# Kernel optimization log

Hardware: AMD Instinct MI355X
Metric: run time of the kernel (lower is better)

## Reference

```python
import jax, jax.numpy as jnp
import numpy as np

B, S, D = 4, 2048, 1024
H, HD = 16, 64  # num_head, head_dim


def setup_inputs() -> dict:
    key = jax.random.key(0)
    k0, k1, k2, k3, k4 = jax.random.split(key, 5)
    scale = 1.0 / np.sqrt(D)
    return {
        "x": jax.random.normal(k0, (B, S, D), dtype=jnp.float32),
        "Wq": jax.random.normal(k1, (D, H * HD), dtype=jnp.float32) * scale,
        "Wk": jax.random.normal(k2, (D, H * HD), dtype=jnp.float32) * scale,
        "Wv": jax.random.normal(k3, (D, H * HD), dtype=jnp.float32) * scale,
        "Wo": jax.random.normal(k4, (H * HD, H * HD), dtype=jnp.float32) * scale,
    }


def reference(x, Wq, Wk, Wv, Wo):
    b, s, _ = x.shape
    # projections -> [b, h, s, hd]
    q = (x @ Wq).reshape(b, s, H, HD).transpose(0, 2, 1, 3)
    k = (x @ Wk).reshape(b, s, H, HD).transpose(0, 2, 1, 3)
    v = (x @ Wv).reshape(b, s, H, HD).transpose(0, 2, 1, 3)
    # scaled scores [b, h, s, s]
    scores = jnp.einsum("bhqd,bhkd->bhqk", q, k) / np.sqrt(HD).astype(np.float32)
    causal = jnp.triu(jnp.ones((s, s), dtype=bool), k=1)  # True above diagonal
    scores = jnp.where(causal, -jnp.inf, scores)
    att = jax.nn.softmax(scores, axis=-1)
    # dropout p=0.0 -> identity
    out = jnp.einsum("bhqk,bhkd->bqhd", att, v).reshape(b, s, H * HD)
    return out @ Wo
```

## Files before the change

kernel.cpp:

```cpp
#include <hip/hip_runtime.h>


typedef __attribute__((ext_vector_type(8))) short short8_t;
typedef __attribute__((ext_vector_type(4))) short short4_t;
typedef __attribute__((ext_vector_type(4))) float float4_t;

constexpr int Bz = 4, Sq = 2048, Dm = 1024, NH = 16, HD = 64;

#define GLOAD_LDS16(g, l)                                                      \
  __builtin_amdgcn_global_load_lds(                                            \
      (const __attribute__((address_space(1))) unsigned int*)(g),              \
      (__attribute__((address_space(3))) unsigned int*)(l), 16, 0, 0)

__device__ __forceinline__ unsigned short f2bf(float f) {
  unsigned u = __builtin_bit_cast(unsigned, f);
  u += 0x7fffu + ((u >> 16) & 1u);
  return (unsigned short)(u >> 16);
}

__device__ __forceinline__ float exp2_fast(float x) {
#if __has_builtin(__builtin_amdgcn_exp2f)
  return __builtin_amdgcn_exp2f(x);
#else
  return exp2f(x);
#endif
}

__device__ __forceinline__ float m3(float a, float b, float c) {
  return fmaxf(fmaxf(a, b), c);
}

__global__ __launch_bounds__(256) void cast_x_kernel(const float* __restrict__ x,
                                                     unsigned short* __restrict__ xb) {
  size_t i = (size_t)blockIdx.x * 256 + threadIdx.x;
  float4 v = ((const float4*)x)[i];
  ushort4 o;
  o.x = f2bf(v.x); o.y = f2bf(v.y); o.z = f2bf(v.z); o.w = f2bf(v.w);
  ((ushort4*)xb)[i] = o;
}

__global__ __launch_bounds__(256) void transpose_w_kernel(
    const float* __restrict__ Wq, const float* __restrict__ Wk,
    const float* __restrict__ Wv, const float* __restrict__ Wo,
    unsigned short* __restrict__ wqT, unsigned short* __restrict__ wkT,
    unsigned short* __restrict__ wvT, unsigned short* __restrict__ woT) {
  __shared__ float tile[64][65];
  int zz = blockIdx.z;
  const float* W = zz == 0 ? Wq : (zz == 1 ? Wk : (zz == 2 ? Wv : Wo));
  unsigned short* WT = zz == 0 ? wqT : (zz == 1 ? wkT : (zz == 2 ? wvT : woT));
  int n0 = blockIdx.x * 64, k0 = blockIdx.y * 64;
  int tx = threadIdx.x & 63, ty = threadIdx.x >> 6;
#pragma unroll
  for (int i = 0; i < 16; ++i) {
    int r = i * 4 + ty;
    tile[r][tx] = W[(size_t)(k0 + r) * Dm + n0 + tx];
  }
  __syncthreads();
#pragma unroll
  for (int i = 0; i < 16; ++i) {
    int r = i * 4 + ty;
    WT[(size_t)(n0 + r) * Dm + k0 + tx] = f2bf(tile[tx][r]);
  }
}

__device__ __forceinline__ void gemm_mainloop(const unsigned short* __restrict__ A,
                                              const unsigned short* __restrict__ BT,
                                              int m0, int n0,
                                              unsigned short* lA, unsigned short* lB,
                                              float4_t acc[4][4]) {
  const int tid = threadIdx.x;
  const int lane = tid & 63, lr = lane & 15, quad = lane >> 4;
  const int wave = tid >> 6;
  const int mw = (wave >> 1) * 64, nw = (wave & 1) * 64;
  const int srow = tid >> 3;
  const int scol = (tid & 7) * 8;
  const unsigned short* ga = A + (size_t)(m0 + srow) * Dm + scol;
  const unsigned short* gb = BT + (size_t)(n0 + srow) * Dm + scol;
  unsigned short* la = lA + tid * 8;
  unsigned short* lb = lB + tid * 8;

  for (int k0 = 0; k0 < Dm; k0 += 64) {
    __syncthreads();
#pragma unroll
    for (int iss = 0; iss < 4; ++iss) {
      GLOAD_LDS16(ga + (size_t)iss * 32 * Dm + k0, la + iss * 32 * 64);
      GLOAD_LDS16(gb + (size_t)iss * 32 * Dm + k0, lb + iss * 32 * 64);
    }
    __syncthreads();
#pragma unroll
    for (int kk = 0; kk < 2; ++kk) {
      short8_t a[4], b[4];
#pragma unroll
      for (int i = 0; i < 4; ++i)
        a[i] = *(const short8_t*)(lA + (mw + i * 16 + lr) * 64 + kk * 32 + quad * 8);
#pragma unroll
      for (int j = 0; j < 4; ++j)
        b[j] = *(const short8_t*)(lB + (nw + j * 16 + lr) * 64 + kk * 32 + quad * 8);
#pragma unroll
      for (int i = 0; i < 4; ++i)
#pragma unroll
        for (int j = 0; j < 4; ++j)
          acc[i][j] = __builtin_amdgcn_mfma_f32_16x16x32_bf16(a[i], b[j], acc[i][j], 0, 0, 0);
    }
  }
}

__global__ __launch_bounds__(256) void gemm_qkv_kernel(
    const unsigned short* __restrict__ xb,
    const unsigned short* __restrict__ wqT, const unsigned short* __restrict__ wkT,
    const unsigned short* __restrict__ wvT,
    unsigned short* __restrict__ qb, unsigned short* __restrict__ kb,
    unsigned short* __restrict__ vt) {
  __shared__ unsigned short lA[128 * 64];
  __shared__ unsigned short lB[128 * 64];
  const unsigned short* WT = blockIdx.z == 0 ? wqT : (blockIdx.z == 1 ? wkT : wvT);
  unsigned short* outb = blockIdx.z == 0 ? qb : (blockIdx.z == 1 ? kb : vt);
  bool isV = blockIdx.z == 2;
  float qscale = (blockIdx.z == 0) ? 0.18033688011112042f : 1.0f;
  int lane = threadIdx.x & 63, wave = threadIdx.x >> 6;
  int lr = lane & 15, quad = lane >> 4;
  int m0 = blockIdx.y * 128, n0 = blockIdx.x * 128;
  int m_base = m0 + (wave >> 1) * 64;
  int n_base = n0 + (wave & 1) * 64;
  float4_t z = {0.f, 0.f, 0.f, 0.f};
  float4_t acc[4][4];
#pragma unroll
  for (int i = 0; i < 4; ++i)
#pragma unroll
    for (int j = 0; j < 4; ++j) acc[i][j] = z;
  gemm_mainloop(xb, WT, m0, n0, lA, lB, acc);
  if (isV) {
#pragma unroll
    for (int i = 0; i < 4; ++i)
#pragma unroll
      for (int j = 0; j < 4; ++j) {
        int m = m_base + i * 16 + quad * 4;
        int n = n_base + j * 16 + lr;
        int b = m >> 11, s = m & (Sq - 1);
        int h = n >> 6, hd = n & (HD - 1);
        ushort4 pk;
        pk.x = f2bf(acc[i][j][0]); pk.y = f2bf(acc[i][j][1]);
        pk.z = f2bf(acc[i][j][2]); pk.w = f2bf(acc[i][j][3]);
        *(ushort4*)(outb + (((size_t)b * NH + h) * HD + hd) * Sq + s) = pk;
      }
  } else {
#pragma unroll
    for (int i = 0; i < 4; ++i)
#pragma unroll
      for (int j = 0; j < 4; ++j)
#pragma unroll
        for (int r = 0; r < 4; ++r) {
          int m = m_base + i * 16 + quad * 4 + r;
          int n = n_base + j * 16 + lr;
          int b = m >> 11, s = m & (Sq - 1);
          int h = n >> 6, hd = n & (HD - 1);
          outb[(((size_t)b * NH + h) * Sq + s) * HD + hd] = f2bf(acc[i][j][r] * qscale);
        }
  }
}

__global__ __launch_bounds__(256) void gemm_out_kernel(
    const unsigned short* __restrict__ ao, const unsigned short* __restrict__ woT,
    float* __restrict__ out) {
  __shared__ unsigned short lA[128 * 64];
  __shared__ unsigned short lB[128 * 64];
  int lane = threadIdx.x & 63, wave = threadIdx.x >> 6;
  int lr = lane & 15, quad = lane >> 4;
  int m0 = blockIdx.y * 128, n0 = blockIdx.x * 128;
  int m_base = m0 + (wave >> 1) * 64;
  int n_base = n0 + (wave & 1) * 64;
  float4_t z = {0.f, 0.f, 0.f, 0.f};
  float4_t acc[4][4];
#pragma unroll
  for (int i = 0; i < 4; ++i)
#pragma unroll
    for (int j = 0; j < 4; ++j) acc[i][j] = z;
  gemm_mainloop(ao, woT, m0, n0, lA, lB, acc);
#pragma unroll
  for (int i = 0; i < 4; ++i)
#pragma unroll
    for (int j = 0; j < 4; ++j)
#pragma unroll
      for (int r = 0; r < 4; ++r) {
        int m = m_base + i * 16 + quad * 4 + r;
        int n = n_base + j * 16 + lr;
        out[(size_t)m * Dm + n] = acc[i][j][r];
      }
}

__global__ __launch_bounds__(256) void attn_kernel(
    const unsigned short* __restrict__ qbuf, const unsigned short* __restrict__ kbuf,
    const unsigned short* __restrict__ vtbuf, unsigned short* __restrict__ ao) {
  __shared__ unsigned short lk[64 * 64];
  __shared__ unsigned short lv[64 * 64];
  int tid = threadIdx.x;
  int bh = blockIdx.x;
  int ti = 31 - (int)blockIdx.y;
  int wave = tid >> 6, lane = tid & 63;
  int lcol = lane & 15, quad = lane >> 4;
  int lc7 = lcol & 7;
  const unsigned short* Q = qbuf + (size_t)bh * Sq * HD;
  const unsigned short* K = kbuf + (size_t)bh * Sq * HD;
  const unsigned short* Vt = vtbuf + (size_t)bh * HD * Sq;
  int b = bh >> 4, h = bh & 15;
  float4_t z = {0.f, 0.f, 0.f, 0.f};

  const int r0 = tid >> 3;
  const int sg = (tid & 7) ^ (r0 & 7);
  const unsigned short* kg_base = K + (size_t)r0 * HD + sg * 8;
  const unsigned short* vg_base = Vt + (size_t)r0 * Sq + sg * 8;
  unsigned short* kl0 = lk + tid * 8;
  unsigned short* kl1 = lk + 2048 + tid * 8;
  unsigned short* vl0 = lv + tid * 8;
  unsigned short* vl1 = lv + 2048 + tid * 8;

  const int koff0 = (quad ^ lc7) * 8;
  const int koff1 = ((quad | 4) ^ lc7) * 8;
  int voff[4];
#pragma unroll
  for (int s4 = 0; s4 < 4; ++s4)
    voff[s4] = (((s4 * 2 + (quad >> 1)) ^ lc7) * 8) + (quad & 1) * 4;

  int q0w = ti * 64 + wave * 16;
  int q_global = q0w + lcol;
  short8_t qf0 = *(const short8_t*)(Q + (size_t)(q0w + lcol) * HD + quad * 8);
  short8_t qf1 = *(const short8_t*)(Q + (size_t)(q0w + lcol) * HD + 32 + quad * 8);
  float m_i = -INFINITY, l_i = 0.f;
  float4_t o[4];
#pragma unroll
  for (int f = 0; f < 4; ++f) o[f] = z;

  int nkt = ti + 1;
  for (int kt = 0; kt < nkt; ++kt) {
    int key0 = kt * 64;
    __syncthreads();
    {
      const unsigned short* kg = kg_base + (size_t)key0 * HD;
      const unsigned short* vg = vg_base + key0;
      GLOAD_LDS16(kg, kl0);
      GLOAD_LDS16(kg + (size_t)32 * HD, kl1);
      GLOAD_LDS16(vg, vl0);
      GLOAD_LDS16(vg + (size_t)32 * Sq, vl1);
    }
    __syncthreads();

    bool need_mask = (key0 + 63 > q0w);
    float s[16];
#pragma unroll
    for (int s4 = 0; s4 < 4; ++s4) {
      const unsigned short* kr = lk + (s4 * 16 + lcol) * 64;
      short8_t kf0 = *(const short8_t*)(kr + koff0);
      short8_t kf1 = *(const short8_t*)(kr + koff1);
      float4_t st = z;
      st = __builtin_amdgcn_mfma_f32_16x16x32_bf16(kf0, qf0, st, 0, 0, 0);
      st = __builtin_amdgcn_mfma_f32_16x16x32_bf16(kf1, qf1, st, 0, 0, 0);
#pragma unroll
      for (int r = 0; r < 4; ++r) {
        float v = st[r];
        if (need_mask && (key0 + s4 * 16 + quad * 4 + r > q_global)) v = -INFINITY;
        s[s4 * 4 + r] = v;
      }
    }
    float ta = m3(s[0], s[1], s[2]);
    float tb = m3(s[3], s[4], s[5]);
    float tc = m3(s[6], s[7], s[8]);
    float td = m3(s[9], s[10], s[11]);
    float te = m3(s[12], s[13], s[14]);
    float tmax = m3(ta, tb, tc);
    tmax = m3(tmax, td, te);
    tmax = fmaxf(tmax, s[15]);
    tmax = fmaxf(tmax, __shfl_xor(tmax, 16, 64));
    tmax = fmaxf(tmax, __shfl_xor(tmax, 32, 64));

    if (__any(tmax > m_i + 8.f)) {
      float m_new = fmaxf(m_i, tmax);
      float alpha = exp2_fast(m_i - m_new);
      l_i *= alpha;
      m_i = m_new;
      float at[4];
#pragma unroll
      for (int r = 0; r < 4; ++r) at[r] = __shfl(alpha, quad * 4 + r, 64);
#pragma unroll
      for (int f = 0; f < 4; ++f)
#pragma unroll
        for (int r = 0; r < 4; ++r) o[f][r] *= at[r];
    }

    float psum = 0.f;
    short4_t pf[4];
#pragma unroll
    for (int s4 = 0; s4 < 4; ++s4) {
      float p0 = exp2_fast(s[s4 * 4 + 0] - m_i);
      float p1 = exp2_fast(s[s4 * 4 + 1] - m_i);
      float p2 = exp2_fast(s[s4 * 4 + 2] - m_i);
      float p3 = exp2_fast(s[s4 * 4 + 3] - m_i);
      psum += (p0 + p1) + (p2 + p3);
      unsigned lo, hi;
      asm("v_cvt_pk_bf16_f32 %0, %1, %2" : "=v"(lo) : "v"(p0), "v"(p1));
      asm("v_cvt_pk_bf16_f32 %0, %1, %2" : "=v"(hi) : "v"(p2), "v"(p3));
      uint2 packed;
      packed.x = lo;
      packed.y = hi;
      pf[s4] = __builtin_bit_cast(short4_t, packed);
    }
    psum += __shfl_xor(psum, 16, 64);
    psum += __shfl_xor(psum, 32, 64);
    l_i += psum;

#pragma unroll
    for (int f = 0; f < 4; ++f) {
      const unsigned short* vr = lv + (f * 16 + lcol) * 64;
#pragma unroll
      for (int s4 = 0; s4 < 4; ++s4) {
        short4_t vf = *(const short4_t*)(vr + voff[s4]);
        o[f] = __builtin_amdgcn_mfma_f32_16x16x16bf16_1k(pf[s4], vf, o[f], 0, 0, 0);
      }
    }
  }

  float lt[4];
#pragma unroll
  for (int r = 0; r < 4; ++r) lt[r] = 1.f / __shfl(l_i, quad * 4 + r, 64);
#pragma unroll
  for (int f = 0; f < 4; ++f)
#pragma unroll
    for (int r = 0; r < 4; ++r) {
      int q = q0w + quad * 4 + r;
      int hd = f * 16 + lcol;
      ao[((size_t)b * Sq + q) * (NH * HD) + h * HD + hd] = f2bf(o[f][r] * lt[r]);
    }
}

extern "C" void kernel_launch(void* const* d_in, const int* in_sizes, int n_in,
                              void* d_out, int out_size, void* d_ws, size_t ws_size,
                              hipStream_t stream) {
  const float* x = (const float*)d_in[0];
  const float* Wq = (const float*)d_in[1];
  const float* Wk = (const float*)d_in[2];
  const float* Wv = (const float*)d_in[3];
  const float* Wo = (const float*)d_in[4];
  float* out = (float*)d_out;

  char* ws = (char*)d_ws;
  size_t off = 0;
  auto carve = [&](size_t bytes) {
    void* p = ws + off;
    off += (bytes + 255) & ~(size_t)255;
    return p;
  };
  const size_t xe = (size_t)Bz * Sq * Dm;
  const size_t we = (size_t)Dm * Dm;
  unsigned short* xb = (unsigned short*)carve(xe * 2);
  unsigned short* wqT = (unsigned short*)carve(we * 2);
  unsigned short* wkT = (unsigned short*)carve(we * 2);
  unsigned short* wvT = (unsigned short*)carve(we * 2);
  unsigned short* woT = (unsigned short*)carve(we * 2);
  unsigned short* qb = (unsigned short*)carve(xe * 2);
  unsigned short* kb = (unsigned short*)carve(xe * 2);
  unsigned short* vt = (unsigned short*)carve(xe * 2);
  unsigned short* ao = (unsigned short*)carve(xe * 2);
  (void)ws_size;

  cast_x_kernel<<<xe / 4 / 256, 256, 0, stream>>>(x, xb);
  transpose_w_kernel<<<dim3(16, 16, 4), 256, 0, stream>>>(Wq, Wk, Wv, Wo,
                                                          wqT, wkT, wvT, woT);
  gemm_qkv_kernel<<<dim3(8, 64, 3), 256, 0, stream>>>(xb, wqT, wkT, wvT, qb, kb, vt);
  attn_kernel<<<dim3(Bz * NH, 32), 256, 0, stream>>>(qb, kb, vt, ao);
  gemm_out_kernel<<<dim3(8, 64), 256, 0, stream>>>(ao, woT, out);
}
```

Before: 280.6 us.

## Double-buffer K/V tiles in attention kernel with register-staged V prefetch

Attention now uses two LDS buffers for K and V, so the next key tile is prefetched while the current one is computed. This replaces the two barriers per iteration with one. K still uses async global-to-LDS loads, while V is loaded into registers early, stored to LDS with a new 8-byte-granularity XOR swizzle, and read with matching offsets. The causal mask is applied only on the diagonal tile. The cost is double the LDS use (which may lower occupancy) and more registers held for the staged V data.

```diff
diff --git a/kernel.cpp b/kernel.cpp
--- a/kernel.cpp
+++ b/kernel.cpp
@@ -191,8 +191,8 @@
 __global__ __launch_bounds__(256) void attn_kernel(
     const unsigned short* __restrict__ qbuf, const unsigned short* __restrict__ kbuf,
     const unsigned short* __restrict__ vtbuf, unsigned short* __restrict__ ao) {
-  __shared__ unsigned short lk[64 * 64];
-  __shared__ unsigned short lv[64 * 64];
+  __shared__ unsigned short lk[2 * 64 * 64];
+  __shared__ unsigned short lv[2 * 64 * 64];
   int tid = threadIdx.x;
   int bh = blockIdx.x;
   int ti = 31 - (int)blockIdx.y;
@@ -206,20 +206,26 @@
   float4_t z = {0.f, 0.f, 0.f, 0.f};
 
   const int r0 = tid >> 3;
-  const int sg = (tid & 7) ^ (r0 & 7);
-  const unsigned short* kg_base = K + (size_t)r0 * HD + sg * 8;
-  const unsigned short* vg_base = Vt + (size_t)r0 * Sq + sg * 8;
-  unsigned short* kl0 = lk + tid * 8;
-  unsigned short* kl1 = lk + 2048 + tid * 8;
-  unsigned short* vl0 = lv + tid * 8;
-  unsigned short* vl1 = lv + 2048 + tid * 8;
+  const int sgk = (tid & 7) ^ (r0 & 7);
+  const unsigned short* kg = K + (size_t)r0 * HD + sgk * 8;
+  const int kdst = tid * 8;
+
+  const int w0 = (tid & 7) * 2;
+  const int xa = r0 & 15;
+  const int d0 = w0 ^ xa;
+  const unsigned short* vsrc = Vt + (size_t)r0 * Sq + w0 * 4;
+  const int vdst = r0 * 64 + d0 * 4;
 
   const int koff0 = (quad ^ lc7) * 8;
   const int koff1 = ((quad | 4) ^ lc7) * 8;
   int voff[4];
 #pragma unroll
-  for (int s4 = 0; s4 < 4; ++s4)
-    voff[s4] = (((s4 * 2 + (quad >> 1)) ^ lc7) * 8) + (quad & 1) * 4;
+  for (int s4 = 0; s4 < 4; ++s4) voff[s4] = ((s4 * 4 + quad) ^ lcol) * 4;
+
+  unsigned short* lkc = lk;
+  unsigned short* lkn = lk + 4096;
+  unsigned short* lvc = lv;
+  unsigned short* lvn = lv + 4096;
 
   int q0w = ti * 64 + wave * 16;
   int q_global = q0w + lcol;
@@ -230,37 +236,56 @@
 #pragma unroll
   for (int f = 0; f < 4; ++f) o[f] = z;
 
+  {
+    GLOAD_LDS16(kg, lkc + kdst);
+    GLOAD_LDS16(kg + (size_t)32 * HD, lkc + 2048 + kdst);
+    short4_t a0 = *(const short4_t*)(vsrc);
+    short4_t a1 = *(const short4_t*)(vsrc + 4);
+    short4_t b0 = *(const short4_t*)(vsrc + (size_t)32 * Sq);
+    short4_t b1 = *(const short4_t*)(vsrc + (size_t)32 * Sq + 4);
+    *(short4_t*)(lvc + vdst) = a0;
+    *(short4_t*)(lvc + (vdst ^ 4)) = a1;
+    *(short4_t*)(lvc + vdst + 2048) = b0;
+    *(short4_t*)(lvc + (vdst ^ 4) + 2048) = b1;
+  }
+  __syncthreads();
+
   int nkt = ti + 1;
   for (int kt = 0; kt < nkt; ++kt) {
-    int key0 = kt * 64;
-    __syncthreads();
-    {
-      const unsigned short* kg = kg_base + (size_t)key0 * HD;
-      const unsigned short* vg = vg_base + key0;
-      GLOAD_LDS16(kg, kl0);
-      GLOAD_LDS16(kg + (size_t)32 * HD, kl1);
-      GLOAD_LDS16(vg, vl0);
-      GLOAD_LDS16(vg + (size_t)32 * Sq, vl1);
-    }
-    __syncthreads();
-
-    bool need_mask = (key0 + 63 > q0w);
+    bool has_next = (kt + 1 < nkt);
+    short4_t a0, a1, b0, b1;
+    if (has_next) {
+      const unsigned short* vs = vsrc + (size_t)(kt + 1) * 64;
+      a0 = *(const short4_t*)(vs);
+      a1 = *(const short4_t*)(vs + 4);
+      b0 = *(const short4_t*)(vs + (size_t)32 * Sq);
+      b1 = *(const short4_t*)(vs + (size_t)32 * Sq + 4);
+      const unsigned short* kgn = kg + (size_t)(kt + 1) * 64 * HD;
+      GLOAD_LDS16(kgn, lkn + kdst);
+      GLOAD_LDS16(kgn + (size_t)32 * HD, lkn + 2048 + kdst);
+    }
+
     float s[16];
 #pragma unroll
     for (int s4 = 0; s4 < 4; ++s4) {
-      const unsigned short* kr = lk + (s4 * 16 + lcol) * 64;
+      const unsigned short* kr = lkc + (s4 * 16 + lcol) * 64;
       short8_t kf0 = *(const short8_t*)(kr + koff0);
       short8_t kf1 = *(const short8_t*)(kr + koff1);
       float4_t st = z;
       st = __builtin_amdgcn_mfma_f32_16x16x32_bf16(kf0, qf0, st, 0, 0, 0);
       st = __builtin_amdgcn_mfma_f32_16x16x32_bf16(kf1, qf1, st, 0, 0, 0);
 #pragma unroll
-      for (int r = 0; r < 4; ++r) {
-        float v = st[r];
-        if (need_mask && (key0 + s4 * 16 + quad * 4 + r > q_global)) v = -INFINITY;
-        s[s4 * 4 + r] = v;
-      }
-    }
+      for (int r = 0; r < 4; ++r) s[s4 * 4 + r] = st[r];
+    }
+    if (kt == ti) {
+      int key0 = kt * 64;
+#pragma unroll
+      for (int s4 = 0; s4 < 4; ++s4)
+#pragma unroll
+        for (int r = 0; r < 4; ++r)
+          if (key0 + s4 * 16 + quad * 4 + r > q_global) s[s4 * 4 + r] = -INFINITY;
+    }
+
     float ta = m3(s[0], s[1], s[2]);
     float tb = m3(s[3], s[4], s[5]);
     float tc = m3(s[6], s[7], s[8]);
@@ -307,15 +332,27 @@
     psum += __shfl_xor(psum, 32, 64);
     l_i += psum;
 
+    if (has_next) {
+      *(short4_t*)(lvn + vdst) = a0;
+      *(short4_t*)(lvn + (vdst ^ 4)) = a1;
+      *(short4_t*)(lvn + vdst + 2048) = b0;
+      *(short4_t*)(lvn + (vdst ^ 4) + 2048) = b1;
+    }
+
 #pragma unroll
     for (int f = 0; f < 4; ++f) {
-      const unsigned short* vr = lv + (f * 16 + lcol) * 64;
+      const unsigned short* vr = lvc + (f * 16 + lcol) * 64;
 #pragma unroll
       for (int s4 = 0; s4 < 4; ++s4) {
         short4_t vf = *(const short4_t*)(vr + voff[s4]);
         o[f] = __builtin_amdgcn_mfma_f32_16x16x16bf16_1k(pf[s4], vf, o[f], 0, 0, 0);
       }
     }
+
+    __syncthreads();
+    unsigned short* t;
+    t = lkc; lkc = lkn; lkn = t;
+    t = lvc; lvc = lvn; lvn = t;
   }
 
   float lt[4];
```

Result: faster. 270.4 us (-3.7%).
